# Performance work log

Measured on AMD Instinct MI355X. Metric: run time of the kernel, lower is better.

## Reference

```python
import jax, jax.numpy as jnp
import numpy as np

B, L, D_MODEL = 2, 2048, 256
D_STATE, D_CONV, EXPAND, HEADDIM = 128, 4, 4, 64
D_INNER = EXPAND * D_MODEL            # 1024
NHEADS = D_INNER // HEADDIM           # 16
CONV_DIM = D_INNER + 2 * D_STATE      # 1280
D_IN_PROJ = 2 * D_INNER + 2 * D_STATE + NHEADS  # 2320
CHUNK = 256
GN_EPS = float(np.finfo(np.float32).eps)
RMS_EPS = 1e-5


def _silu(x):
    return x * jax.nn.sigmoid(x)


def _segsum(x):
    # x: (..., T) -> (..., T, T); out[i, j] = sum_{j<k<=i} x[k] for i>=j else -inf
    T = x.shape[-1]
    cs = jnp.cumsum(x, -1)
    d = cs[..., :, None] - cs[..., None, :]
    mask = jnp.tril(jnp.ones((T, T), bool))
    return jnp.where(mask, d, -jnp.inf)


def _ssd(X, A, Bm, Cm):
    # Chunked SSD (Mamba2 ssd_minimal_discrete). X:(b,l,h,p) already dt-scaled,
    # A:(b,l,h) = dt * (-exp(A_log)), Bm/Cm:(b,l,n) with ngroups=1.
    b, l, h, p = X.shape
    c = l // CHUNK
    Xc = X.reshape(b, c, CHUNK, h, p)
    Ac = jnp.transpose(A.reshape(b, c, CHUNK, h), (0, 3, 1, 2))  # (b,h,c,Q)
    Bc = Bm.reshape(b, c, CHUNK, -1)
    Cc = Cm.reshape(b, c, CHUNK, -1)
    A_cs = jnp.cumsum(Ac, -1)                                    # (b,h,c,Q)
    Lmat = jnp.exp(_segsum(Ac))                                  # (b,h,c,Q,Q)
    CB = jnp.einsum('bcln,bcsn->bcls', Cc, Bc)                   # (b,c,Q,Q)
    Y_diag = jnp.einsum('bhcls,bcshp->bclhp', Lmat * CB[:, None], Xc)
    decay_states = jnp.exp(A_cs[..., -1:] - A_cs)                # (b,h,c,Q)
    states = jnp.einsum('bcln,bhcl,bclhp->bchpn', Bc, decay_states, Xc)
    states = jnp.concatenate([jnp.zeros_like(states[:, :1]), states], 1)  # (b,c+1,h,p,n)
    decay_chunk = jnp.exp(_segsum(jnp.pad(A_cs[..., -1], ((0, 0), (0, 0), (1, 0)))))  # (b,h,c+1,c+1)
    new_states = jnp.einsum('bhzc,bchpn->bzhpn', decay_chunk, states)[:, :-1]
    state_decay = jnp.exp(A_cs)                                  # (b,h,c,Q)
    Y_off = jnp.einsum('bcln,bchpn,bhcl->bclhp', Cc, new_states, state_decay)
    return (Y_diag + Y_off).reshape(b, l, h, p)


def _mamba2(u, in_w, conv_w, conv_b, dt_bias, A_log, Dh, norm_w, out_w):
    # u: (b, l, d_model)
    b, l, _ = u.shape
    zxbcdt = u @ in_w.T                                          # (b,l,D_IN_PROJ)
    z = zxbcdt[..., :D_INNER]
    xBC = zxbcdt[..., D_INNER:D_INNER + CONV_DIM]
    dt = jax.nn.softplus(zxbcdt[..., -NHEADS:] + dt_bias)        # (b,l,h)
    # causal depthwise conv over time
    xc = jnp.transpose(xBC, (0, 2, 1))                           # (b,C,l)
    xc = jax.lax.conv_general_dilated(xc, conv_w, (1,), [(D_CONV - 1, 0)],
                                      dimension_numbers=('NCH', 'OIH', 'NCH'),
                                      feature_group_count=CONV_DIM)
    xBC = _silu(jnp.transpose(xc + conv_b[None, :, None], (0, 2, 1)))
    x = xBC[..., :D_INNER].reshape(b, l, NHEADS, HEADDIM)
    Bm = xBC[..., D_INNER:D_INNER + D_STATE]
    Cm = xBC[..., D_INNER + D_STATE:]
    A = dt * (-jnp.exp(A_log))                                   # (b,l,h)
    y = _ssd(dt[..., None] * x, A, Bm, Cm) + x * Dh[None, None, :, None]
    y = y.reshape(b, l, D_INNER) * _silu(z)                      # gated
    y = y * jax.lax.rsqrt(jnp.mean(y * y, -1, keepdims=True) + RMS_EPS) * norm_w
    return y @ out_w.T                                           # (b,l,d_model)


def _resmamba(x, gn_w, gn_b, fp, bp, proj_w, proj_b):
    # GroupNorm(1, C) over (C, L) per sample
    mu = jnp.mean(x, (1, 2), keepdims=True)
    var = jnp.mean((x - mu) ** 2, (1, 2), keepdims=True)
    xn = (x - mu) * jax.lax.rsqrt(var + GN_EPS) * gn_w[None, :, None] + gn_b[None, :, None]
    t = jnp.transpose(xn, (0, 2, 1))                             # (B,L,C)
    fwd = _mamba2(t, *fp)
    bwd = jnp.flip(_mamba2(jnp.flip(t, 1), *bp), 1)
    r = jnp.concatenate([fwd + t, bwd + t], -1)                  # (B,L,2C)
    pr = r @ proj_w.T + proj_b                                   # (B,L,C)
    return x + jnp.transpose(pr, (0, 2, 1))


def setup_inputs():
    key = jax.random.key(0)
    ks = jax.random.split(key, 4)
    s = 0.02
    inp = {
        'x': jax.random.normal(ks[0], (B, D_MODEL, L), jnp.float32),
        'gn_w': jnp.ones((D_MODEL,), jnp.float32),
        'gn_b': jnp.zeros((D_MODEL,), jnp.float32),
        'proj_w': s * jax.random.normal(ks[1], (D_MODEL, 2 * D_MODEL), jnp.float32),
        'proj_b': jnp.zeros((D_MODEL,), jnp.float32),
    }
    for i, p in enumerate(('f', 'b')):
        kk = jax.random.split(ks[2 + i], 5)
        inp[p + '_in_w'] = s * jax.random.normal(kk[0], (D_IN_PROJ, D_MODEL), jnp.float32)
        inp[p + '_conv_w'] = s * jax.random.normal(kk[1], (CONV_DIM, 1, D_CONV), jnp.float32)
        inp[p + '_conv_b'] = jnp.zeros((CONV_DIM,), jnp.float32)
        inp[p + '_dt_bias'] = 0.1 * jax.random.normal(kk[2], (NHEADS,), jnp.float32)
        inp[p + '_A_log'] = jnp.log(jax.random.uniform(kk[3], (NHEADS,), jnp.float32, 1.0, 16.0))
        inp[p + '_D'] = jnp.ones((NHEADS,), jnp.float32)
        inp[p + '_norm_w'] = jnp.ones((D_INNER,), jnp.float32)
        inp[p + '_out_w'] = s * jax.random.normal(kk[4], (D_MODEL, D_INNER), jnp.float32)
    return inp


def reference(x, gn_w, gn_b, proj_w, proj_b,
              f_in_w, f_conv_w, f_conv_b, f_dt_bias, f_A_log, f_D, f_norm_w, f_out_w,
              b_in_w, b_conv_w, b_conv_b, b_dt_bias, b_A_log, b_D, b_norm_w, b_out_w):
    fp = (f_in_w, f_conv_w, f_conv_b, f_dt_bias, f_A_log, f_D, f_norm_w, f_out_w)
    bp = (b_in_w, b_conv_w, b_conv_b, b_dt_bias, b_A_log, b_D, b_norm_w, b_out_w)
    return _resmamba(x, gn_w, gn_b, fp, bp, proj_w, proj_b)
```

## Files before the change

kernel.cpp:

```cpp
#include <hip/hip_runtime.h>
#include <hip/hip_bf16.h>
#include <math.h>

using bf16 = __hip_bfloat16;

#define L_SEQ   2048
#define DMODEL  256
#define DINNER  1024
#define DSTATE  128
#define NH      16
#define HD      64
#define CONVDIM 1280
#define DPROJ   2320
#define NCHK    8
#define CT      256
#define BATCH   2
#define M_TOT   (BATCH*L_SEQ)

#define ACS_N   (BATCH*NH*NCHK*CT)
#define ST_N    ((size_t)BATCH*NCHK*NH*HD*DSTATE)
#define CB_N    ((size_t)BATCH*NCHK*CT*CT)

typedef __bf16 bf16x8_t __attribute__((ext_vector_type(8)));
typedef __bf16 bf16x4_t __attribute__((ext_vector_type(4)));
typedef float  f32x4_t  __attribute__((ext_vector_type(4)));

__device__ __forceinline__ float tof(bf16 v){ return __bfloat162float(v); }
__device__ __forceinline__ bf16  tob(float v){ return __float2bfloat16(v); }
__device__ __forceinline__ float expdec(float a){ return __expf(fminf(a, 0.f)); }

struct CastJob  { const float* src; bf16* dst; int n; };
struct CastJobs { CastJob j[3]; };

__global__ __launch_bounds__(256) void k_cast5(CastJobs jobs){
  CastJob jb = jobs.j[blockIdx.y];
  int i = (blockIdx.x*256 + threadIdx.x)*4;
  if (i < jb.n){
    float4 v = *(const float4*)(jb.src + i);
    jb.dst[i]   = tob(v.x); jb.dst[i+1] = tob(v.y);
    jb.dst[i+2] = tob(v.z); jb.dst[i+3] = tob(v.w);
  }
}

__global__ __launch_bounds__(256) void k_prep(const float* __restrict__ ow0, const float* __restrict__ ow1,
                                              const float* __restrict__ pw,
                                              bf16* __restrict__ owt, bf16* __restrict__ psum){
  int bz = blockIdx.x;
  int t = threadIdx.x;
  if (bz < 128){
    int dir = bz >> 6; int tid = bz & 63;
    int k0 = (tid >> 2)*64, j0 = (tid & 3)*64;
    const float* src = dir ? ow1 : ow0;
    bf16* dst = owt + (size_t)dir*DINNER*DMODEL;
    __shared__ __bf16 tile[64][65];
    #pragma unroll
    for (int it = 0; it < 2; ++it){
      int idx = t + it*256; int jj = idx >> 3; int k8 = (idx & 7)*8;
      float4 va = *(const float4*)&src[(size_t)(j0+jj)*DINNER + k0 + k8];
      float4 vb = *(const float4*)&src[(size_t)(j0+jj)*DINNER + k0 + k8 + 4];
      tile[k8+0][jj] = (__bf16)va.x; tile[k8+1][jj] = (__bf16)va.y;
      tile[k8+2][jj] = (__bf16)va.z; tile[k8+3][jj] = (__bf16)va.w;
      tile[k8+4][jj] = (__bf16)vb.x; tile[k8+5][jj] = (__bf16)vb.y;
      tile[k8+6][jj] = (__bf16)vb.z; tile[k8+7][jj] = (__bf16)vb.w;
    }
    __syncthreads();
    #pragma unroll
    for (int it = 0; it < 2; ++it){
      int idx = t + it*256; int kr = idx >> 3; int j8 = (idx & 7)*8;
      bf16x8_t o;
      #pragma unroll
      for (int i = 0; i < 8; ++i) o[i] = tile[kr][j8+i];
      *(bf16x8_t*)&dst[(size_t)(k0+kr)*DMODEL + j0 + j8] = o;
    }
  } else {
    int i = ((bz - 128)*256 + t)*8;
    int n = i >> 8, j = i & 255;
    const float* row = pw + (size_t)n*(2*DMODEL);
    bf16x8_t o;
    #pragma unroll
    for (int c = 0; c < 8; ++c) o[c] = (__bf16)(row[j+c] + row[256+j+c]);
    *(bf16x8_t*)&psum[i] = o;
  }
}

__global__ __launch_bounds__(256) void k_stats1(const float* __restrict__ x, float2* __restrict__ pbuf){
  int b = blockIdx.y, blk = blockIdx.x, t = threadIdx.x;
  const float4* p = (const float4*)(x + (size_t)b*(DMODEL*L_SEQ) + (size_t)blk*4096);
  float s = 0.f, ss = 0.f;
  #pragma unroll
  for (int k = 0; k < 4; ++k){
    float4 v = p[t + k*256];
    s  += v.x + v.y + v.z + v.w;
    ss += v.x*v.x + v.y*v.y + v.z*v.z + v.w*v.w;
  }
  for (int o = 32; o > 0; o >>= 1){ s += __shfl_down(s, o, 64); ss += __shfl_down(ss, o, 64); }
  __shared__ float sh[8];
  if ((t & 63) == 0){ sh[(t>>6)*2] = s; sh[(t>>6)*2+1] = ss; }
  __syncthreads();
  if (t == 0){
    s  = sh[0]+sh[2]+sh[4]+sh[6];
    ss = sh[1]+sh[3]+sh[5]+sh[7];
    pbuf[b*128 + blk] = make_float2(s, ss);
  }
}

__global__ __launch_bounds__(128) void k_stats2(const float2* __restrict__ pbuf, float* __restrict__ stats){
  int b = blockIdx.x, t = threadIdx.x;
  float2 v = pbuf[b*128 + t];
  float s = v.x, ss = v.y;
  for (int o = 32; o > 0; o >>= 1){ s += __shfl_down(s, o, 64); ss += __shfl_down(ss, o, 64); }
  __shared__ float sh[4];
  if ((t & 63) == 0){ sh[(t>>6)*2] = s; sh[(t>>6)*2+1] = ss; }
  __syncthreads();
  if (t == 0){
    s  = sh[0]+sh[2];
    ss = sh[1]+sh[3];
    float inv = 1.f/(float)(DMODEL*L_SEQ);
    float mu = s*inv, var = ss*inv - mu*mu;
    stats[0 + b*2] = mu; stats[1 + b*2] = rsqrtf(fmaxf(var, 0.f) + 1.1920929e-07f);
  }
}

__global__ __launch_bounds__(256) void k_t(const float* __restrict__ x, const float* __restrict__ gw,
                                           const float* __restrict__ gb, const float* __restrict__ stats,
                                           bf16* __restrict__ t_out){
  __shared__ float tile[64][65];
  int l0 = blockIdx.x*64, c0 = blockIdx.y*64, b = blockIdx.z;
  float mu = stats[b*2], istd = stats[b*2+1];
  int tid = threadIdx.x;
  int lx = tid & 63, cy = tid >> 6;
  for (int cc = cy; cc < 64; cc += 4){
    float v = x[(size_t)b*DMODEL*L_SEQ + (size_t)(c0+cc)*L_SEQ + l0+lx];
    tile[cc][lx] = (v - mu)*istd;
  }
  __syncthreads();
  int cx = tid & 63, ly = tid >> 6;
  float w = gw[c0+cx], bb = gb[c0+cx];
  for (int ll = ly; ll < 64; ll += 4)
    t_out[((size_t)(b*L_SEQ) + l0+ll)*DMODEL + c0+cx] = tob(tile[cx][ll]*w + bb);
}

template<class Epi>
__global__ __launch_bounds__(256) void gemm_epi(const bf16* __restrict__ A, int lda,
                                                const bf16* __restrict__ B, int ldb,
                                                int M, int N, int K, Epi epi){
  __shared__ __align__(16) bf16 lds[2][(128+128)*40];
  int dir = blockIdx.z;
  const bf16* Bd = B + (size_t)dir*(size_t)N*ldb;
  int orig = blockIdx.x;
  int swz = (orig & 7)*76 + (orig >> 3);
  int m0 = (swz & 31)*128;
  int n0 = (swz >> 5)*128;
  int t = threadIdx.x;
  int wave = t >> 6, lane = t & 63;
  int wm = (wave & 1)*64, wn = (wave >> 1)*64;
  int lrow = lane & 15, quad = lane >> 4, lk8 = quad*8;

  int r0 = t >> 2, o0 = (t & 3)*8;
  int r1 = r0 + 64;
  int am0 = m0 + r0, am1 = m0 + r1;
  if (dir){
    am0 = (am0 & ~(L_SEQ-1)) | ((L_SEQ-1) - (am0 & (L_SEQ-1)));
    am1 = (am1 & ~(L_SEQ-1)) | ((L_SEQ-1) - (am1 & (L_SEQ-1)));
  }
  int bn0 = n0 + r0; if (bn0 > N-1) bn0 = N-1;
  int bn1 = n0 + r1; if (bn1 > N-1) bn1 = N-1;
  const bf16* Ap0 = A + (size_t)am0*lda + o0;
  const bf16* Ap1 = A + (size_t)am1*lda + o0;
  const bf16* Bp0 = Bd + (size_t)bn0*ldb + o0;
  const bf16* Bp1 = Bd + (size_t)bn1*ldb + o0;

  f32x4_t acc[4][4];
  #pragma unroll
  for (int i = 0; i < 4; ++i)
    #pragma unroll
    for (int j = 0; j < 4; ++j) acc[i][j] = (f32x4_t){0,0,0,0};

  int nit = K >> 5;
  uint4 a0 = *(const uint4*)Ap0;
  uint4 a1 = *(const uint4*)Ap1;
  uint4 b0 = *(const uint4*)Bp0;
  uint4 b1 = *(const uint4*)Bp1;
  int st = 0;
  *(uint4*)&lds[0][r0*40 + o0] = a0;
  *(uint4*)&lds[0][r1*40 + o0] = a1;
  *(uint4*)&lds[0][(128 + r0)*40 + o0] = b0;
  *(uint4*)&lds[0][(128 + r1)*40 + o0] = b1;
  __syncthreads();
  for (int it = 0; it < nit; ++it){
    bool more = (it+1 < nit);
    if (more){
      int kk = (it+1) << 5;
      a0 = *(const uint4*)(Ap0 + kk);
      a1 = *(const uint4*)(Ap1 + kk);
      b0 = *(const uint4*)(Bp0 + kk);
      b1 = *(const uint4*)(Bp1 + kk);
    }
    const bf16* cs = lds[st];
    bf16x8_t bfr[4];
    #pragma unroll
    for (int ni = 0; ni < 4; ++ni) bfr[ni] = *(const bf16x8_t*)&cs[(128 + wn + ni*16 + lrow)*40 + lk8];
    #pragma unroll
    for (int mi = 0; mi < 4; ++mi){
      bf16x8_t af = *(const bf16x8_t*)&cs[(wm + mi*16 + lrow)*40 + lk8];
      #pragma unroll
      for (int ni = 0; ni < 4; ++ni)
        acc[mi][ni] = __builtin_amdgcn_mfma_f32_16x16x32_bf16(af, bfr[ni], acc[mi][ni], 0, 0, 0);
    }
    if (more){
      st ^= 1;
      *(uint4*)&lds[st][r0*40 + o0] = a0;
      *(uint4*)&lds[st][r1*40 + o0] = a1;
      *(uint4*)&lds[st][(128 + r0)*40 + o0] = b0;
      *(uint4*)&lds[st][(128 + r1)*40 + o0] = b1;
      __syncthreads();
    }
  }
  #pragma unroll
  for (int mi = 0; mi < 4; ++mi)
    #pragma unroll
    for (int ni = 0; ni < 4; ++ni)
      #pragma unroll
      for (int r = 0; r < 4; ++r){
        int m = m0 + wm + mi*16 + quad*4 + r;
        int n = n0 + wn + ni*16 + lrow;
        if (m < M && n < N) epi(dir, m, n, acc[mi][ni][r]);
      }
}

struct EpiInProj {
  bf16* z; bf16* xbc; float* dt; const float* db0; const float* db1;
  __device__ void operator()(int dir, int m, int n, float v) const {
    size_t mm = (size_t)dir*M_TOT + m;
    if (n < DINNER) z[mm*DINNER + n] = tob(v);
    else if (n < DINNER+CONVDIM) xbc[mm*CONVDIM + (n-DINNER)] = tob(v);
    else {
      int h = n - (DINNER+CONVDIM);
      float xx = v + (dir ? db1 : db0)[h];
      dt[mm*NH + h] = (xx > 20.f) ? xx : log1pf(expf(xx));
    }
  }
};

__global__ __launch_bounds__(256) void gemm_w(const bf16* __restrict__ P, const bf16* __restrict__ owt,
                                              bf16* __restrict__ W){
  __shared__ __align__(16) bf16 lds[2][(128+64)*40];
  int dir = blockIdx.z;
  int m0 = blockIdx.x*128, n0 = blockIdx.y*64;
  int t = threadIdx.x;
  int wave = t >> 6, lane = t & 63;
  int wm = (wave & 1)*64, wn = (wave >> 1)*32;
  int lrow = lane & 15, quad = lane >> 4, lk8 = quad*8;

  int r0 = t >> 2, o0 = (t & 3)*8;
  int r1 = r0 + 64;
  const bf16* Ap0 = P + (size_t)(m0 + r0)*(2*DMODEL) + dir*DMODEL + o0;
  const bf16* Ap1 = P + (size_t)(m0 + r1)*(2*DMODEL) + dir*DMODEL + o0;
  const bf16* Bp  = owt + (size_t)dir*DINNER*DMODEL + (size_t)(n0 + r0)*DMODEL + o0;

  f32x4_t acc[4][2];
  #pragma unroll
  for (int i = 0; i < 4; ++i){ acc[i][0] = (f32x4_t){0,0,0,0}; acc[i][1] = (f32x4_t){0,0,0,0}; }

  int nit = DMODEL >> 5;
  uint4 a0 = *(const uint4*)Ap0;
  uint4 a1 = *(const uint4*)Ap1;
  uint4 b0 = *(const uint4*)Bp;
  int st = 0;
  *(uint4*)&lds[0][r0*40 + o0] = a0;
  *(uint4*)&lds[0][r1*40 + o0] = a1;
  *(uint4*)&lds[0][(128 + r0)*40 + o0] = b0;
  __syncthreads();
  for (int it = 0; it < nit; ++it){
    bool more = (it+1 < nit);
    if (more){
      int kk = (it+1) << 5;
      a0 = *(const uint4*)(Ap0 + kk);
      a1 = *(const uint4*)(Ap1 + kk);
      b0 = *(const uint4*)(Bp + kk);
    }
    const bf16* cs = lds[st];
    bf16x8_t af[4], bfr[2];
    #pragma unroll
    for (int mi = 0; mi < 4; ++mi) af[mi] = *(const bf16x8_t*)&cs[(wm + mi*16 + lrow)*40 + lk8];
    #pragma unroll
    for (int ni = 0; ni < 2; ++ni) bfr[ni] = *(const bf16x8_t*)&cs[(128 + wn + ni*16 + lrow)*40 + lk8];
    #pragma unroll
    for (int mi = 0; mi < 4; ++mi)
      #pragma unroll
      for (int ni = 0; ni < 2; ++ni)
        acc[mi][ni] = __builtin_amdgcn_mfma_f32_16x16x32_bf16(af[mi], bfr[ni], acc[mi][ni], 0, 0, 0);
    if (more){
      st ^= 1;
      *(uint4*)&lds[st][r0*40 + o0] = a0;
      *(uint4*)&lds[st][r1*40 + o0] = a1;
      *(uint4*)&lds[st][(128 + r0)*40 + o0] = b0;
      __syncthreads();
    }
  }
  bf16* Wd = W + (size_t)dir*DMODEL*DINNER;
  #pragma unroll
  for (int mi = 0; mi < 4; ++mi)
    #pragma unroll
    for (int ni = 0; ni < 2; ++ni)
      #pragma unroll
      for (int r = 0; r < 4; ++r){
        int m = m0 + wm + mi*16 + quad*4 + r;
        int n = n0 + wn + ni*16 + lrow;
        Wd[(size_t)m*DINNER + n] = tob(acc[mi][ni][r]);
      }
}

__global__ __launch_bounds__(256) void gemm_final(const bf16* __restrict__ y, const bf16* __restrict__ tb,
                                                  const bf16* __restrict__ W, const bf16* __restrict__ psum,
                                                  const float* __restrict__ x, const float* __restrict__ pb,
                                                  float* __restrict__ out){
  __shared__ __align__(16) bf16 lds[2][(32+64)*40];
  __shared__ float tile[32][65];
  int orig = blockIdx.x;
  int swz = (orig & 7)*64 + (orig >> 3);
  int mt_ = swz & 127, nt_ = swz >> 7;
  int m0 = mt_*32, n0 = nt_*64;
  int t = threadIdx.x;
  int wave = t >> 6, lane = t & 63;
  int lrow = lane & 15, quad = lane >> 4, lk8 = quad*8;
  int wn = wave*16;

  f32x4_t acc[2];
  acc[0] = (f32x4_t){0,0,0,0}; acc[1] = (f32x4_t){0,0,0,0};

  int rA = t >> 2, oA = (t & 3)*8;

  #pragma unroll
  for (int ph = 0; ph < 3; ++ph){
    const bf16 *Ab, *Bb; int lda, ldb, K, rev;
    if (ph == 0){ Ab = y;                             lda = DINNER; K = DINNER; Bb = W;                             ldb = DINNER; rev = 0; }
    else if (ph == 1){ Ab = y + (size_t)M_TOT*DINNER; lda = DINNER; K = DINNER; Bb = W + (size_t)DMODEL*DINNER;     ldb = DINNER; rev = 1; }
    else { Ab = tb; lda = DMODEL; K = DMODEL; Bb = psum; ldb = DMODEL; rev = 0; }

    int am = m0 + rA;
    if (rev) am = (am & ~(L_SEQ-1)) | ((L_SEQ-1) - (am & (L_SEQ-1)));
    const bf16* Ap = Ab + (size_t)am*lda + oA;
    const bf16* Bp = Bb + (size_t)(n0 + rA)*ldb + oA;

    int nit = K >> 5;
    uint4 a0, b0;
    if (t < 128) a0 = *(const uint4*)Ap;
    b0 = *(const uint4*)Bp;
    __syncthreads();
    int st = 0;
    if (t < 128) *(uint4*)&lds[0][rA*40 + oA] = a0;
    *(uint4*)&lds[0][(32 + rA)*40 + oA] = b0;
    __syncthreads();
    for (int it = 0; it < nit; ++it){
      bool more = (it+1 < nit);
      if (more){
        int kk = (it+1) << 5;
        if (t < 128) a0 = *(const uint4*)(Ap + kk);
        b0 = *(const uint4*)(Bp + kk);
      }
      const bf16* cs = lds[st];
      bf16x8_t bq = *(const bf16x8_t*)&cs[(32 + wn + lrow)*40 + lk8];
      #pragma unroll
      for (int mt = 0; mt < 2; ++mt){
        bf16x8_t af = *(const bf16x8_t*)&cs[(mt*16 + lrow)*40 + lk8];
        acc[mt] = __builtin_amdgcn_mfma_f32_16x16x32_bf16(af, bq, acc[mt], 0, 0, 0);
      }
      if (more){
        st ^= 1;
        if (t < 128) *(uint4*)&lds[st][rA*40 + oA] = a0;
        *(uint4*)&lds[st][(32 + rA)*40 + oA] = b0;
        __syncthreads();
      }
    }
  }

  #pragma unroll
  for (int mt = 0; mt < 2; ++mt)
    #pragma unroll
    for (int r = 0; r < 4; ++r)
      tile[mt*16 + quad*4 + r][wn + lrow] = acc[mt][r];
  __syncthreads();
  int b = m0 >> 11, l0 = m0 & (L_SEQ-1);
  int tx = t & 31, ny = t >> 5;
  for (int nn = ny; nn < 64; nn += 8){
    int n = n0 + nn;
    size_t xi = (size_t)b*DMODEL*L_SEQ + (size_t)n*L_SEQ + l0 + tx;
    out[xi] = tile[tx][nn] + pb[n] + x[xi];
  }
}

__global__ __launch_bounds__(256) void k_conv(const bf16* __restrict__ xraw, const float* __restrict__ cw0,
                                              const float* __restrict__ cb0, const float* __restrict__ cw1,
                                              const float* __restrict__ cb1, bf16* __restrict__ xconv){
  int t = threadIdx.x;
  int tx = t & 31, ty = t >> 5;
  int ch0 = blockIdx.x*256 + tx*8;
  int z = blockIdx.z; int b = z & 1, dir = z >> 1;
  int lbase = blockIdx.y*32 + ty*4;
  const float* cw = dir ? cw1 : cw0;
  const float* cb = dir ? cb1 : cb0;
  const bf16* xr = xraw  + (size_t)dir*((size_t)M_TOT*CONVDIM) + (size_t)(b*L_SEQ)*CONVDIM + ch0;
  bf16* xcv      = xconv + (size_t)dir*((size_t)M_TOT*CONVDIM) + (size_t)(b*L_SEQ)*CONVDIM + ch0;

  float wk[4][8];
  #pragma unroll
  for (int c = 0; c < 8; ++c){
    float4 w = *(const float4*)&cw[(ch0+c)*4];
    wk[0][c] = w.x; wk[1][c] = w.y; wk[2][c] = w.z; wk[3][c] = w.w;
  }
  float bias[8];
  {
    float4 b0v = *(const float4*)&cb[ch0];
    float4 b1v = *(const float4*)&cb[ch0+4];
    bias[0]=b0v.x; bias[1]=b0v.y; bias[2]=b0v.z; bias[3]=b0v.w;
    bias[4]=b1v.x; bias[5]=b1v.y; bias[6]=b1v.z; bias[7]=b1v.w;
  }

  bf16x8_t zero;
  #pragma unroll
  for (int c = 0; c < 8; ++c) zero[c] = (__bf16)0.f;

  bf16x8_t win[4];
  #pragma unroll
  for (int k = 0; k < 3; ++k){
    int ls = lbase - 3 + k;
    win[k] = (ls >= 0) ? *(const bf16x8_t*)&xr[(size_t)ls*CONVDIM] : zero;
  }
  #pragma unroll
  for (int i = 0; i < 4; ++i){
    int l = lbase + i;
    win[3] = *(const bf16x8_t*)&xr[(size_t)l*CONVDIM];
    bf16x8_t outv;
    #pragma unroll
    for (int c = 0; c < 8; ++c){
      float a = bias[c] + (float)win[0][c]*wk[0][c] + (float)win[1][c]*wk[1][c]
                        + (float)win[2][c]*wk[2][c] + (float)win[3][c]*wk[3][c];
      outv[c] = (__bf16)(a / (1.f + __expf(-a)));
    }
    *(bf16x8_t*)&xcv[(size_t)l*CONVDIM] = outv;
    win[0] = win[1]; win[1] = win[2]; win[2] = win[3];
  }
}

__global__ __launch_bounds__(256) void k_states(const bf16* __restrict__ xconv, const float* __restrict__ dt,
                                                const float* __restrict__ Al0, const float* __restrict__ Al1,
                                                float* __restrict__ A_cs, float* __restrict__ states){
  int id0 = blockIdx.x;
  int dir = id0 >> 8; int id = id0 & 255;
  int h = id & 15; int bc = id >> 4; int ch = bc & 7; int b = bc >> 3;
  int t = threadIdx.x;
  __shared__ float s_acs[CT];
  __shared__ float w_s[CT];
  __shared__ __align__(16) __bf16 Xt[64*72];
  __shared__ __align__(16) __bf16 Bt[128*72];
  const bf16* xc = xconv + (size_t)dir*((size_t)M_TOT*CONVDIM);
  const float* dtp = dt + (size_t)dir*((size_t)M_TOT*NH);
  const float* Alog = dir ? Al1 : Al0;
  size_t rowbase = (size_t)(b*L_SEQ) + ch*CT;

  float dtv = dtp[(rowbase + t)*NH + h];
  s_acs[t] = -expf(Alog[h]) * dtv;
  __syncthreads();
  for (int off = 1; off < 256; off <<= 1){
    float v = (t >= off) ? s_acs[t-off] : 0.f;
    __syncthreads();
    s_acs[t] += v;
    __syncthreads();
  }
  A_cs[(size_t)dir*ACS_N + (size_t)((b*NH+h)*NCHK + ch)*CT + t] = s_acs[t];
  float alast = s_acs[CT-1];
  w_s[t] = dtv * __expf(fminf(alast - s_acs[t], 0.f));
  __syncthreads();

  int wave = t >> 6, lane = t & 63, lrow = lane & 15, quad = lane >> 4;
  f32x4_t acc[8];
  #pragma unroll
  for (int i = 0; i < 8; ++i) acc[i] = (f32x4_t){0.f,0.f,0.f,0.f};

  for (int kt = 0; kt < 4; ++kt){
    int l0 = kt*64;
    #pragma unroll
    for (int it = 0; it < 2; ++it){
      int idx = t + it*256; int l = idx >> 3; int p0 = (idx & 7)*8;
      bf16x8_t v = *(const bf16x8_t*)&xc[(rowbase + l0 + l)*CONVDIM + h*HD + p0];
      float w = w_s[l0 + l];
      int col = (((l>>3) ^ ((p0>>3)&7))<<3) | (l&7);
      #pragma unroll
      for (int j = 0; j < 8; ++j) Xt[(p0+j)*72 + col] = (__bf16)((float)v[j]*w);
    }
    #pragma unroll
    for (int it = 0; it < 4; ++it){
      int idx = t + it*256; int l = idx >> 4; int n0 = (idx & 15)*8;
      bf16x8_t v = *(const bf16x8_t*)&xc[(rowbase + l0 + l)*CONVDIM + DINNER + n0];
      int col = (((l>>3) ^ ((n0>>3)&7))<<3) | (l&7);
      #pragma unroll
      for (int j = 0; j < 8; ++j) Bt[(n0+j)*72 + col] = v[j];
    }
    __syncthreads();
    int arow = wave*16 + lrow;
    #pragma unroll
    for (int ks = 0; ks < 2; ++ks){
      int kg = ks*4 + quad;
      bf16x8_t af = *(const bf16x8_t*)&Xt[arow*72 + ((kg ^ ((arow>>3)&7))<<3)];
      #pragma unroll
      for (int nt = 0; nt < 8; ++nt){
        int brow = nt*16 + lrow;
        bf16x8_t bq = *(const bf16x8_t*)&Bt[brow*72 + ((kg ^ ((brow>>3)&7))<<3)];
        acc[nt] = __builtin_amdgcn_mfma_f32_16x16x32_bf16(af, bq, acc[nt], 0, 0, 0);
      }
    }
    __syncthreads();
  }
  float* so = states + (size_t)dir*ST_N + (size_t)id*HD*DSTATE;
  int m = wave*16 + quad*4;
  #pragma unroll
  for (int nt = 0; nt < 8; ++nt)
    #pragma unroll
    for (int r = 0; r < 4; ++r)
      so[(size_t)(m+r)*DSTATE + nt*16 + lrow] = acc[nt][r];
}

__global__ __launch_bounds__(256) void k_recur(float* __restrict__ states, const float* __restrict__ A_cs){
  int blk = blockIdx.x;
  int bh2 = blk >> 5;
  int e = (blk & 31)*256 + threadIdx.x;
  int dir = bh2 >> 5; int bh = bh2 & 31;
  int h = bh & 15, b = bh >> 4;
  const float* ac = A_cs + (size_t)dir*ACS_N;
  float* st = states + (size_t)dir*ST_N;
  float s = 0.f;
  #pragma unroll
  for (int ch = 0; ch < NCHK; ++ch){
    float dec = expdec(ac[((size_t)(bh*NCHK+ch))*CT + CT-1]);
    size_t off = (size_t)(((b*NCHK+ch)*NH)+h)*HD*DSTATE + e;
    float cur = st[off];
    st[off] = s;
    s = s*dec + cur;
  }
}

__global__ __launch_bounds__(256) void k_cb(const bf16* __restrict__ xconv, float* __restrict__ CB){
  int zz = blockIdx.z;
  int dir = zz >> 4; int b = (zz >> 3) & 1; int ch = zz & 7;
  int m0 = blockIdx.x*64, n0 = blockIdx.y*64;
  if (n0 > m0) return;
  const bf16* base = xconv + (size_t)dir*((size_t)M_TOT*CONVDIM) + (size_t)(b*L_SEQ + ch*CT)*CONVDIM;
  const bf16* Crow = base + DINNER + DSTATE;
  const bf16* Brow = base + DINNER;
  __shared__ __align__(16) __bf16 As[64*136];
  __shared__ __align__(16) __bf16 Bs[64*136];
  int t = threadIdx.x;
  int r = t >> 2, o0 = (t & 3)*32;
  #pragma unroll
  for (int j = 0; j < 4; ++j){
    *(bf16x8_t*)&As[r*136 + o0 + j*8] = *(const bf16x8_t*)&Crow[(size_t)(m0+r)*CONVDIM + o0 + j*8];
    *(bf16x8_t*)&Bs[r*136 + o0 + j*8] = *(const bf16x8_t*)&Brow[(size_t)(n0+r)*CONVDIM + o0 + j*8];
  }
  __syncthreads();
  int wave = t >> 6, lane = t & 63, lrow = lane & 15, quad = lane >> 4;
  int wm = wave*16;
  f32x4_t acc[4];
  #pragma unroll
  for (int i = 0; i < 4; ++i) acc[i] = (f32x4_t){0.f,0.f,0.f,0.f};
  #pragma unroll
  for (int ks = 0; ks < 4; ++ks){
    bf16x8_t af = *(const bf16x8_t*)&As[(wm+lrow)*136 + ks*32 + quad*8];
    #pragma unroll
    for (int nt = 0; nt < 4; ++nt){
      bf16x8_t bq = *(const bf16x8_t*)&Bs[(nt*16+lrow)*136 + ks*32 + quad*8];
      acc[nt] = __builtin_amdgcn_mfma_f32_16x16x32_bf16(af, bq, acc[nt], 0, 0, 0);
    }
  }
  float* outp = CB + (size_t)dir*CB_N + (size_t)(b*NCHK+ch)*CT*CT;
  #pragma unroll
  for (int nt = 0; nt < 4; ++nt)
    #pragma unroll
    for (int r2 = 0; r2 < 4; ++r2)
      outp[(size_t)(m0+wm+quad*4+r2)*CT + n0+nt*16+lrow] = acc[nt][r2];
}

__global__ __launch_bounds__(256) void k_y_mfma(const bf16* __restrict__ xconv, const float* __restrict__ dt,
                                                const float* __restrict__ A_cs, const float* __restrict__ CB,
                                                const float* __restrict__ ns, bf16* __restrict__ y){
  int id0 = blockIdx.x;
  int dir = id0 >> 9; int id = id0 & 511;
  int hh = id & 1; int r = id >> 1; int h = r & 15; int bc = r >> 4; int ch = bc & 7; int b = bc >> 3;
  int t = threadIdx.x;
  int lane = t & 63;
  int lrow = lane & 15, quad = lane >> 4;

  __shared__ __align__(16) bf16 Xs[64*264];
  __shared__ __align__(16) bf16 NSs[64*136];
  __shared__ float acs_s[CT];

  const bf16* xc = xconv + (size_t)dir*((size_t)M_TOT*CONVDIM);
  const float* dtp = dt + (size_t)dir*((size_t)M_TOT*NH);
  const float* acs = A_cs + (size_t)dir*ACS_N + (size_t)((b*NH+h)*NCHK + ch)*CT;
  const float* cbz = CB + (size_t)dir*CB_N + (size_t)(b*NCHK+ch)*CT*CT;
  const float* nsp = ns + (size_t)dir*ST_N + (size_t)(((b*NCHK+ch)*NH)+h)*HD*DSTATE;
  bf16* yp = y + (size_t)dir*((size_t)M_TOT*DINNER);
  size_t rowbase = (size_t)(b*L_SEQ + ch*CT);
  acs_s[t] = acs[t];

  #pragma unroll
  for (int it = 0; it < 8; ++it){
    int idx = t + it*256;
    int s = idx >> 3, p0 = (idx & 7)*8;
    float dtv = dtp[(rowbase + s)*NH + h];
    bf16x8_t v = *(const bf16x8_t*)&xc[(rowbase + s)*CONVDIM + h*HD + p0];
    int col = ((((s>>3) ^ ((p0>>3)&7)))<<3) | (s&7);
    #pragma unroll
    for (int j = 0; j < 8; ++j)
      Xs[(p0+j)*264 + col] = tob((float)v[j] * dtv);
  }
  for (int it = 0; it < 8; ++it){
    int idx = t + it*256;
    int n4 = (idx & 31)*4, p = idx >> 5;
    float4 v = *(const float4*)(nsp + p*DSTATE + n4);
    bf16* w = &NSs[p*136 + n4];
    w[0] = tob(v.x); w[1] = tob(v.y); w[2] = tob(v.z); w[3] = tob(v.w);
  }
  __syncthreads();

  int wave = t >> 6;
  int row0 = hh*128 + wave*32;
  float al0 = acs_s[row0 + lrow];
  float al1 = acs_s[row0 + 16 + lrow];
  float acs_r0 = acs_s[row0];

  f32x4_t acc[2][4];
  #pragma unroll
  for (int i = 0; i < 2; ++i)
    #pragma unroll
    for (int j = 0; j < 4; ++j) acc[i][j] = (f32x4_t){0.f,0.f,0.f,0.f};

  int nst = (row0 + 32) >> 5;
  for (int st = 0; st < nst; ++st){
    int s0 = st*32;
    if (s0 + 31 < row0 && (acs_r0 - acs_s[s0+31]) < -30.f) continue;
    int sg = (s0 >> 3) + quad;
    bf16x8_t bq[4];
    #pragma unroll
    for (int nt = 0; nt < 4; ++nt){
      int brow = nt*16 + lrow;
      bq[nt] = *(const bf16x8_t*)&Xs[brow*264 + ((sg ^ ((brow>>3)&7))<<3)];
    }
    bf16x8_t af[2];
    #pragma unroll
    for (int mt = 0; mt < 2; ++mt){
      int l = row0 + mt*16 + lrow;
      float al = mt ? al1 : al0;
      const float* cbrow = cbz + (size_t)l*CT + s0 + quad*8;
      float4 c0 = *(const float4*)cbrow;
      float4 c1 = *(const float4*)(cbrow + 4);
      float cv[8] = {c0.x,c0.y,c0.z,c0.w,c1.x,c1.y,c1.z,c1.w};
      union { bf16x8_t v; __bf16 e[8]; } wa;
      #pragma unroll
      for (int j = 0; j < 8; ++j){
        int s = s0 + quad*8 + j;
        float w = (s <= l) ? __expf(fminf(al - acs_s[s], 0.f)) * cv[j] : 0.f;
        wa.e[j] = (__bf16)w;
      }
      af[mt] = wa.v;
    }
    #pragma unroll
    for (int mt = 0; mt < 2; ++mt)
      #pragma unroll
      for (int nt = 0; nt < 4; ++nt)
        acc[mt][nt] = __builtin_amdgcn_mfma_f32_16x16x32_bf16(af[mt], bq[nt], acc[mt][nt], 0, 0, 0);
  }

  float el0 = __expf(fminf(al0, 0.f));
  float el1 = __expf(fminf(al1, 0.f));
  #pragma unroll
  for (int kt = 0; kt < 4; ++kt){
    int n0 = kt*32;
    bf16x8_t bq[4];
    #pragma unroll
    for (int nt = 0; nt < 4; ++nt)
      bq[nt] = *(const bf16x8_t*)&NSs[(nt*16+lrow)*136 + n0 + quad*8];
    bf16x8_t af[2];
    #pragma unroll
    for (int mt = 0; mt < 2; ++mt){
      int l = row0 + mt*16 + lrow;
      float el = mt ? el1 : el0;
      union { bf16x8_t v; __bf16 e[8]; } cu;
      cu.v = *(const bf16x8_t*)&xc[(rowbase + l)*CONVDIM + DINNER + DSTATE + n0 + quad*8];
      union { bf16x8_t v; __bf16 e[8]; } wa;
      #pragma unroll
      for (int j = 0; j < 8; ++j) wa.e[j] = (__bf16)((float)cu.e[j] * el);
      af[mt] = wa.v;
    }
    #pragma unroll
    for (int mt = 0; mt < 2; ++mt)
      #pragma unroll
      for (int nt = 0; nt < 4; ++nt)
        acc[mt][nt] = __builtin_amdgcn_mfma_f32_16x16x32_bf16(af[mt], bq[nt], acc[mt][nt], 0, 0, 0);
  }

  #pragma unroll
  for (int mt = 0; mt < 2; ++mt)
    #pragma unroll
    for (int nt = 0; nt < 4; ++nt)
      #pragma unroll
      for (int rr = 0; rr < 4; ++rr){
        int l = row0 + mt*16 + quad*4 + rr;
        int p = nt*16 + lrow;
        yp[(rowbase + l)*DINNER + h*HD + p] = tob(acc[mt][nt][rr]);
      }
}

__global__ __launch_bounds__(256) void k_gaterms(const bf16* __restrict__ z, const float* __restrict__ nw0,
                                                 const float* __restrict__ nw1, const bf16* __restrict__ xconv,
                                                 const float* __restrict__ Dh0, const float* __restrict__ Dh1,
                                                 bf16* __restrict__ y){
  int m0 = blockIdx.x;
  int dir = m0 >> 12; int m = m0 & (M_TOT-1);
  int t = threadIdx.x;
  const float* nw = dir ? nw1 : nw0;
  const float* Dh = dir ? Dh1 : Dh0;
  int j0 = t*4;
  const bf16* zp = z + (size_t)dir*((size_t)M_TOT*DINNER) + (size_t)m*DINNER;
  const bf16* xc = xconv + (size_t)dir*((size_t)M_TOT*CONVDIM) + (size_t)m*CONVDIM;
  bf16* yp = y + (size_t)dir*((size_t)M_TOT*DINNER) + (size_t)m*DINNER;

  bf16x4_t zv = *(const bf16x4_t*)&zp[j0];
  bf16x4_t yv = *(const bf16x4_t*)&yp[j0];
  bf16x4_t xv = *(const bf16x4_t*)&xc[j0];
  float Dv = Dh[j0 >> 6];
  float v[4]; float ss = 0.f;
  #pragma unroll
  for (int c = 0; c < 4; ++c){
    float zf = (float)zv[c];
    float raw = (float)yv[c] + Dv*(float)xv[c];
    float g = raw * (zf / (1.f + __expf(-zf)));
    v[c] = g; ss += g*g;
  }
  for (int o = 32; o > 0; o >>= 1) ss += __shfl_down(ss, o, 64);
  __shared__ float sh[4];
  if ((t & 63) == 0) sh[t>>6] = ss;
  __syncthreads();
  ss = sh[0]+sh[1]+sh[2]+sh[3];
  float scale = rsqrtf(ss*(1.f/DINNER) + 1e-5f);
  float4 nwv = *(const float4*)&nw[j0];
  float nws[4] = {nwv.x, nwv.y, nwv.z, nwv.w};
  bf16x4_t o;
  #pragma unroll
  for (int c = 0; c < 4; ++c) o[c] = (__bf16)(v[c]*scale*nws[c]);
  *(bf16x4_t*)&yp[j0] = o;
}

extern "C" void kernel_launch(void* const* d_in, const int* in_sizes, int n_in,
                              void* d_out, int out_size, void* d_ws, size_t ws_size,
                              hipStream_t stream){
  (void)in_sizes; (void)n_in; (void)out_size; (void)ws_size;
  const float* x      = (const float*)d_in[0];
  const float* gn_w   = (const float*)d_in[1];
  const float* gn_b   = (const float*)d_in[2];
  const float* proj_w = (const float*)d_in[3];
  const float* proj_b = (const float*)d_in[4];
  float* out = (float*)d_out;

  char* wp = (char*)d_ws;
  auto alloc = [&](size_t bytes){ void* r = (void*)wp; wp += (bytes + 255) & ~(size_t)255; return r; };
  bf16*  t_buf  = (bf16*) alloc((size_t)M_TOT*DMODEL*2);
  bf16*  z_buf  = (bf16*) alloc((size_t)2*M_TOT*DINNER*2);
  bf16*  xraw   = (bf16*) alloc((size_t)2*M_TOT*CONVDIM*2);
  bf16*  xconv  = (bf16*) alloc((size_t)2*M_TOT*CONVDIM*2);
  float* dt_buf = (float*)alloc((size_t)2*M_TOT*NH*4);
  float* acs    = (float*)alloc((size_t)2*ACS_N*4);
  float* states = (float*)alloc((size_t)2*ST_N*4);
  float* cb     = (float*)alloc((size_t)2*CB_N*4);
  float* stats  = (float*)alloc(16);
  float2* pbuf  = (float2*)alloc(BATCH*128*sizeof(float2));
  bf16*  inw_bf   = (bf16*)alloc((size_t)2*DPROJ*DMODEL*2);
  bf16*  projw_bf = (bf16*)alloc((size_t)DMODEL*2*DMODEL*2);
  bf16*  owt      = (bf16*)alloc((size_t)2*DINNER*DMODEL*2);
  bf16*  wfb      = (bf16*)alloc((size_t)2*DMODEL*DINNER*2);
  bf16*  psum     = (bf16*)alloc((size_t)DMODEL*DMODEL*2);
  bf16*  y_buf    = xraw;

  CastJobs jobs;
  jobs.j[0] = { (const float*)d_in[5],  inw_bf,                        DPROJ*DMODEL };
  jobs.j[1] = { (const float*)d_in[13], inw_bf + (size_t)DPROJ*DMODEL, DPROJ*DMODEL };
  jobs.j[2] = { proj_w,                 projw_bf,                      DMODEL*2*DMODEL };
  k_cast5<<<dim3(DPROJ*DMODEL/4/256, 3), 256, 0, stream>>>(jobs);

  k_prep<<<160, 256, 0, stream>>>((const float*)d_in[12], (const float*)d_in[20], proj_w, owt, psum);
  gemm_w<<<dim3(2, 16, 2), 256, 0, stream>>>(projw_bf, owt, wfb);

  k_stats1<<<dim3(128, BATCH), 256, 0, stream>>>(x, pbuf);
  k_stats2<<<BATCH, 128, 0, stream>>>(pbuf, stats);
  k_t<<<dim3(32,4,2), 256, 0, stream>>>(x, gn_w, gn_b, stats, t_buf);

  EpiInProj e1{z_buf, xraw, dt_buf, (const float*)d_in[8], (const float*)d_in[16]};
  gemm_epi<EpiInProj><<<dim3(608, 1, 2), 256, 0, stream>>>(
      t_buf, DMODEL, inw_bf, DMODEL, M_TOT, DPROJ, DMODEL, e1);

  k_conv<<<dim3(5, L_SEQ/32, 2*BATCH), 256, 0, stream>>>(
      xraw, (const float*)d_in[6], (const float*)d_in[7],
            (const float*)d_in[14], (const float*)d_in[15], xconv);
  k_states<<<2*BATCH*NCHK*NH, 256, 0, stream>>>(
      xconv, dt_buf, (const float*)d_in[9], (const float*)d_in[17], acs, states);
  k_recur<<<2*BATCH*NH*32, 256, 0, stream>>>(states, acs);
  k_cb<<<dim3(4,4,2*BATCH*NCHK), 256, 0, stream>>>(xconv, cb);
  k_y_mfma<<<2*BATCH*NCHK*NH*2, 256, 0, stream>>>(xconv, dt_buf, acs, cb, states, y_buf);
  k_gaterms<<<2*M_TOT, 256, 0, stream>>>(
      z_buf, (const float*)d_in[11], (const float*)d_in[19], xconv,
      (const float*)d_in[10], (const float*)d_in[18], y_buf);

  gemm_final<<<512, 256, 0, stream>>>(y_buf, t_buf, wfb, psum, x, proj_b, out);
}
```

Before: 252.7 us.

## Merge front-end prep kernels and fold stats reduction; widen k_y_mfma blocks

Fuses the weight casts, out-proj transpose, proj weight sum and first-stage GroupNorm stats into a single k_front launch, and moves the second-stage stats reduction into k_t so each block recomputes mean/istd from the partial sums. This removes three kernel launches and their serialization gaps. k_y_mfma now uses 512-thread blocks covering a whole chunk-head, so X and state tiles are loaded into LDS once instead of twice across two half-blocks. The cost is lower occupancy and fewer blocks for the y kernel, plus a small redundant reduction in every k_t block.

New measurement: 240.0 us. -5.0%, faster.

```diff
diff --git a/kernel.cpp b/kernel.cpp
--- a/kernel.cpp
+++ b/kernel.cpp
@@ -29,30 +29,34 @@
 __device__ __forceinline__ bf16  tob(float v){ return __float2bfloat16(v); }
 __device__ __forceinline__ float expdec(float a){ return __expf(fminf(a, 0.f)); }
 
-struct CastJob  { const float* src; bf16* dst; int n; };
-struct CastJobs { CastJob j[3]; };
-
-__global__ __launch_bounds__(256) void k_cast5(CastJobs jobs){
-  CastJob jb = jobs.j[blockIdx.y];
-  int i = (blockIdx.x*256 + threadIdx.x)*4;
-  if (i < jb.n){
-    float4 v = *(const float4*)(jb.src + i);
-    jb.dst[i]   = tob(v.x); jb.dst[i+1] = tob(v.y);
-    jb.dst[i+2] = tob(v.z); jb.dst[i+3] = tob(v.w);
-  }
-}
-
-__global__ __launch_bounds__(256) void k_prep(const float* __restrict__ ow0, const float* __restrict__ ow1,
-                                              const float* __restrict__ pw,
-                                              bf16* __restrict__ owt, bf16* __restrict__ psum){
-  int bz = blockIdx.x;
-  int t = threadIdx.x;
-  if (bz < 128){
-    int dir = bz >> 6; int tid = bz & 63;
+__global__ __launch_bounds__(256) void k_front(
+    const float* __restrict__ iw0, const float* __restrict__ iw1, const float* __restrict__ pw,
+    bf16* __restrict__ inw_bf, bf16* __restrict__ projw_bf,
+    const float* __restrict__ ow0, const float* __restrict__ ow1,
+    bf16* __restrict__ owt, bf16* __restrict__ psum,
+    const float* __restrict__ x, float2* __restrict__ pbuf){
+  __shared__ __bf16 tile[64][65];
+  __shared__ float sh[8];
+  int bz = blockIdx.x, t = threadIdx.x;
+  if (bz < 1160){
+    int dir = bz >= 580; int sub = dir ? bz - 580 : bz;
+    const float* src = dir ? iw1 : iw0;
+    bf16* dst = inw_bf + (size_t)dir*DPROJ*DMODEL;
+    int i = (sub*256 + t)*4;
+    float4 v = *(const float4*)(src + i);
+    dst[i]   = tob(v.x); dst[i+1] = tob(v.y);
+    dst[i+2] = tob(v.z); dst[i+3] = tob(v.w);
+  } else if (bz < 1288){
+    int i = ((bz-1160)*256 + t)*4;
+    float4 v = *(const float4*)(pw + i);
+    projw_bf[i]   = tob(v.x); projw_bf[i+1] = tob(v.y);
+    projw_bf[i+2] = tob(v.z); projw_bf[i+3] = tob(v.w);
+  } else if (bz < 1416){
+    int sub = bz - 1288;
+    int dir = sub >> 6; int tid = sub & 63;
     int k0 = (tid >> 2)*64, j0 = (tid & 3)*64;
     const float* src = dir ? ow1 : ow0;
     bf16* dst = owt + (size_t)dir*DINNER*DMODEL;
-    __shared__ __bf16 tile[64][65];
     #pragma unroll
     for (int it = 0; it < 2; ++it){
       int idx = t + it*256; int jj = idx >> 3; int k8 = (idx & 7)*8;
@@ -72,62 +76,53 @@
       for (int i = 0; i < 8; ++i) o[i] = tile[kr][j8+i];
       *(bf16x8_t*)&dst[(size_t)(k0+kr)*DMODEL + j0 + j8] = o;
     }
-  } else {
-    int i = ((bz - 128)*256 + t)*8;
-    int n = i >> 8, j = i & 255;
-    const float* row = pw + (size_t)n*(2*DMODEL);
+  } else if (bz < 1448){
+    int i = ((bz - 1416)*256 + t)*8;
+    int j = i & 255;
+    const float* row = pw + (size_t)(i >> 8)*(2*DMODEL);
     bf16x8_t o;
     #pragma unroll
     for (int c = 0; c < 8; ++c) o[c] = (__bf16)(row[j+c] + row[256+j+c]);
     *(bf16x8_t*)&psum[i] = o;
-  }
-}
-
-__global__ __launch_bounds__(256) void k_stats1(const float* __restrict__ x, float2* __restrict__ pbuf){
-  int b = blockIdx.y, blk = blockIdx.x, t = threadIdx.x;
-  const float4* p = (const float4*)(x + (size_t)b*(DMODEL*L_SEQ) + (size_t)blk*4096);
-  float s = 0.f, ss = 0.f;
-  #pragma unroll
-  for (int k = 0; k < 4; ++k){
-    float4 v = p[t + k*256];
-    s  += v.x + v.y + v.z + v.w;
-    ss += v.x*v.x + v.y*v.y + v.z*v.z + v.w*v.w;
-  }
-  for (int o = 32; o > 0; o >>= 1){ s += __shfl_down(s, o, 64); ss += __shfl_down(ss, o, 64); }
-  __shared__ float sh[8];
-  if ((t & 63) == 0){ sh[(t>>6)*2] = s; sh[(t>>6)*2+1] = ss; }
-  __syncthreads();
-  if (t == 0){
-    s  = sh[0]+sh[2]+sh[4]+sh[6];
-    ss = sh[1]+sh[3]+sh[5]+sh[7];
-    pbuf[b*128 + blk] = make_float2(s, ss);
-  }
-}
-
-__global__ __launch_bounds__(128) void k_stats2(const float2* __restrict__ pbuf, float* __restrict__ stats){
-  int b = blockIdx.x, t = threadIdx.x;
-  float2 v = pbuf[b*128 + t];
-  float s = v.x, ss = v.y;
-  for (int o = 32; o > 0; o >>= 1){ s += __shfl_down(s, o, 64); ss += __shfl_down(ss, o, 64); }
-  __shared__ float sh[4];
-  if ((t & 63) == 0){ sh[(t>>6)*2] = s; sh[(t>>6)*2+1] = ss; }
-  __syncthreads();
-  if (t == 0){
-    s  = sh[0]+sh[2];
-    ss = sh[1]+sh[3];
-    float inv = 1.f/(float)(DMODEL*L_SEQ);
-    float mu = s*inv, var = ss*inv - mu*mu;
-    stats[0 + b*2] = mu; stats[1 + b*2] = rsqrtf(fmaxf(var, 0.f) + 1.1920929e-07f);
+  } else {
+    int sub = bz - 1448;
+    int blk = sub & 127, b = sub >> 7;
+    const float4* p = (const float4*)(x + (size_t)b*(DMODEL*L_SEQ) + (size_t)blk*4096);
+    float s = 0.f, ss = 0.f;
+    #pragma unroll
+    for (int k = 0; k < 4; ++k){
+      float4 v = p[t + k*256];
+      s  += v.x + v.y + v.z + v.w;
+      ss += v.x*v.x + v.y*v.y + v.z*v.z + v.w*v.w;
+    }
+    for (int o = 32; o > 0; o >>= 1){ s += __shfl_down(s, o, 64); ss += __shfl_down(ss, o, 64); }
+    if ((t & 63) == 0){ sh[(t>>6)*2] = s; sh[(t>>6)*2+1] = ss; }
+    __syncthreads();
+    if (t == 0){
+      s  = sh[0]+sh[2]+sh[4]+sh[6];
+      ss = sh[1]+sh[3]+sh[5]+sh[7];
+      pbuf[b*128 + blk] = make_float2(s, ss);
+    }
   }
 }
 
 __global__ __launch_bounds__(256) void k_t(const float* __restrict__ x, const float* __restrict__ gw,
-                                           const float* __restrict__ gb, const float* __restrict__ stats,
+                                           const float* __restrict__ gb, const float2* __restrict__ pbuf,
                                            bf16* __restrict__ t_out){
   __shared__ float tile[64][65];
+  __shared__ float sh[4];
   int l0 = blockIdx.x*64, c0 = blockIdx.y*64, b = blockIdx.z;
-  float mu = stats[b*2], istd = stats[b*2+1];
   int tid = threadIdx.x;
+  float s = 0.f, ss = 0.f;
+  if (tid < 128){ float2 v = pbuf[b*128 + tid]; s = v.x; ss = v.y; }
+  for (int o = 32; o > 0; o >>= 1){ s += __shfl_down(s, o, 64); ss += __shfl_down(ss, o, 64); }
+  if (tid < 128 && (tid & 63) == 0){ sh[(tid>>6)*2] = s; sh[(tid>>6)*2+1] = ss; }
+  __syncthreads();
+  float inv = 1.f/(float)(DMODEL*L_SEQ);
+  float s0 = sh[0]+sh[2], ss0 = sh[1]+sh[3];
+  float mu = s0*inv, var = ss0*inv - mu*mu;
+  float istd = rsqrtf(fmaxf(var, 0.f) + 1.1920929e-07f);
+
   int lx = tid & 63, cy = tid >> 6;
   for (int cc = cy; cc < 64; cc += 4){
     float v = x[(size_t)b*DMODEL*L_SEQ + (size_t)(c0+cc)*L_SEQ + l0+lx];
@@ -580,12 +575,12 @@
       outp[(size_t)(m0+wm+quad*4+r2)*CT + n0+nt*16+lrow] = acc[nt][r2];
 }
 
-__global__ __launch_bounds__(256) void k_y_mfma(const bf16* __restrict__ xconv, const float* __restrict__ dt,
+__global__ __launch_bounds__(512) void k_y_mfma(const bf16* __restrict__ xconv, const float* __restrict__ dt,
                                                 const float* __restrict__ A_cs, const float* __restrict__ CB,
                                                 const float* __restrict__ ns, bf16* __restrict__ y){
   int id0 = blockIdx.x;
-  int dir = id0 >> 9; int id = id0 & 511;
-  int hh = id & 1; int r = id >> 1; int h = r & 15; int bc = r >> 4; int ch = bc & 7; int b = bc >> 3;
+  int dir = id0 >> 8; int id = id0 & 255;
+  int h = id & 15; int bc = id >> 4; int ch = bc & 7; int b = bc >> 3;
   int t = threadIdx.x;
   int lane = t & 63;
   int lrow = lane & 15, quad = lane >> 4;
@@ -601,11 +596,11 @@
   const float* nsp = ns + (size_t)dir*ST_N + (size_t)(((b*NCHK+ch)*NH)+h)*HD*DSTATE;
   bf16* yp = y + (size_t)dir*((size_t)M_TOT*DINNER);
   size_t rowbase = (size_t)(b*L_SEQ + ch*CT);
-  acs_s[t] = acs[t];
-
-  #pragma unroll
-  for (int it = 0; it < 8; ++it){
-    int idx = t + it*256;
+  if (t < CT) acs_s[t] = acs[t];
+
+  #pragma unroll
+  for (int it = 0; it < 4; ++it){
+    int idx = t + it*512;
     int s = idx >> 3, p0 = (idx & 7)*8;
     float dtv = dtp[(rowbase + s)*NH + h];
     bf16x8_t v = *(const bf16x8_t*)&xc[(rowbase + s)*CONVDIM + h*HD + p0];
@@ -614,8 +609,8 @@
     for (int j = 0; j < 8; ++j)
       Xs[(p0+j)*264 + col] = tob((float)v[j] * dtv);
   }
-  for (int it = 0; it < 8; ++it){
-    int idx = t + it*256;
+  for (int it = 0; it < 4; ++it){
+    int idx = t + it*512;
     int n4 = (idx & 31)*4, p = idx >> 5;
     float4 v = *(const float4*)(nsp + p*DSTATE + n4);
     bf16* w = &NSs[p*136 + n4];
@@ -624,7 +619,7 @@
   __syncthreads();
 
   int wave = t >> 6;
-  int row0 = hh*128 + wave*32;
+  int row0 = wave*32;
   float al0 = acs_s[row0 + lrow];
   float al1 = acs_s[row0 + 16 + lrow];
   float acs_r0 = acs_s[row0];
@@ -772,7 +767,6 @@
   float* acs    = (float*)alloc((size_t)2*ACS_N*4);
   float* states = (float*)alloc((size_t)2*ST_N*4);
   float* cb     = (float*)alloc((size_t)2*CB_N*4);
-  float* stats  = (float*)alloc(16);
   float2* pbuf  = (float2*)alloc(BATCH*128*sizeof(float2));
   bf16*  inw_bf   = (bf16*)alloc((size_t)2*DPROJ*DMODEL*2);
   bf16*  projw_bf = (bf16*)alloc((size_t)DMODEL*2*DMODEL*2);
@@ -781,18 +775,15 @@
   bf16*  psum     = (bf16*)alloc((size_t)DMODEL*DMODEL*2);
   bf16*  y_buf    = xraw;
 
-  CastJobs jobs;
-  jobs.j[0] = { (const float*)d_in[5],  inw_bf,                        DPROJ*DMODEL };
-  jobs.j[1] = { (const float*)d_in[13], inw_bf + (size_t)DPROJ*DMODEL, DPROJ*DMODEL };
-  jobs.j[2] = { proj_w,                 projw_bf,                      DMODEL*2*DMODEL };
-  k_cast5<<<dim3(DPROJ*DMODEL/4/256, 3), 256, 0, stream>>>(jobs);
-
-  k_prep<<<160, 256, 0, stream>>>((const float*)d_in[12], (const float*)d_in[20], proj_w, owt, psum);
+  k_front<<<1704, 256, 0, stream>>>(
+      (const float*)d_in[5], (const float*)d_in[13], proj_w,
+      inw_bf, projw_bf,
+      (const float*)d_in[12], (const float*)d_in[20], owt, psum,
+      x, pbuf);
+
   gemm_w<<<dim3(2, 16, 2), 256, 0, stream>>>(projw_bf, owt, wfb);
 
-  k_stats1<<<dim3(128, BATCH), 256, 0, stream>>>(x, pbuf);
-  k_stats2<<<BATCH, 128, 0, stream>>>(pbuf, stats);
-  k_t<<<dim3(32,4,2), 256, 0, stream>>>(x, gn_w, gn_b, stats, t_buf);
+  k_t<<<dim3(32,4,2), 256, 0, stream>>>(x, gn_w, gn_b, pbuf, t_buf);
 
   EpiInProj e1{z_buf, xraw, dt_buf, (const float*)d_in[8], (const float*)d_in[16]};
   gemm_epi<EpiInProj><<<dim3(608, 1, 2), 256, 0, stream>>>(
@@ -805,7 +796,7 @@
       xconv, dt_buf, (const float*)d_in[9], (const float*)d_in[17], acs, states);
   k_recur<<<2*BATCH*NH*32, 256, 0, stream>>>(states, acs);
   k_cb<<<dim3(4,4,2*BATCH*NCHK), 256, 0, stream>>>(xconv, cb);
-  k_y_mfma<<<2*BATCH*NCHK*NH*2, 256, 0, stream>>>(xconv, dt_buf, acs, cb, states, y_buf);
+  k_y_mfma<<<2*BATCH*NCHK*NH, 512, 0, stream>>>(xconv, dt_buf, acs, cb, states, y_buf);
   k_gaterms<<<2*M_TOT, 256, 0, stream>>>(
       z_buf, (const float*)d_in[11], (const float*)d_in[19], xconv,
       (const float*)d_in[10], (const float*)d_in[18], y_buf);
```
